# Kernel tuning notes

Measured on AMD Instinct MI355X. Metric: run time of the kernel, lower is better.

## Reference

```python
import jax, jax.numpy as jnp
import numpy as np

N_NODES = 100000
NEG_SLOPE = 0.2  # PyG GATConv default LeakyReLU slope


def gat_conv(x, W, att_src, att_dst, bias, edge_index, num_nodes, concat):
    """PyG-style GATConv with default add_self_loops=True.
    x: [N, Fin], W: [Fin, H*C], att_src/att_dst: [H, C], bias: [H*C] or [C].
    """
    H, C = att_src.shape
    h = (x @ W).reshape(num_nodes, H, C)              # [N, H, C]
    # append self-loops (PyG default)
    loops = jnp.arange(num_nodes, dtype=edge_index.dtype)
    src = jnp.concatenate([edge_index[0], loops])     # [E+N]
    dst = jnp.concatenate([edge_index[1], loops])
    # per-node attention logits, then per-edge score
    a_src = jnp.sum(h * att_src[None], axis=-1)       # [N, H]
    a_dst = jnp.sum(h * att_dst[None], axis=-1)       # [N, H]
    e = jax.nn.leaky_relu(a_src[src] + a_dst[dst], NEG_SLOPE)  # [E+N, H]
    # softmax over incoming edges of each destination node
    m = jax.ops.segment_max(e, dst, num_segments=num_nodes)    # [N, H]
    e = jnp.exp(e - m[dst])
    denom = jax.ops.segment_sum(e, dst, num_segments=num_nodes)
    alpha = e / denom[dst]                                      # [E+N, H]
    # scatter-aggregate weighted source features
    msg = h[src] * alpha[..., None]                             # [E+N, H, C]
    out = jax.ops.segment_sum(msg, dst, num_segments=num_nodes)  # [N, H, C]
    if concat:
        out = out.reshape(num_nodes, H * C)
    else:
        out = out.mean(axis=1)
    return out + bias


def setup_inputs() -> dict:
    key = jax.random.key(0)
    ks = jax.random.split(key, 12)
    N, E = N_NODES, 1600000
    Fin, Ch, Hh, Cout = 128, 64, 2, 64

    def glorot(k, shape):
        fan = shape[0] + shape[-1]
        return jax.random.uniform(k, shape, jnp.float32, -1.0, 1.0) * np.sqrt(6.0 / fan)

    x = jax.random.normal(ks[0], (N, Fin), jnp.float32)
    edge_index = jax.random.randint(ks[1], (2, E), 0, N, jnp.int32)
    W1 = glorot(ks[2], (Fin, Hh * Ch))
    att_src1 = glorot(ks[3], (Hh, Ch))
    att_dst1 = glorot(ks[4], (Hh, Ch))
    b1 = jnp.zeros((Hh * Ch,), jnp.float32)
    W2 = glorot(ks[5], (Hh * Ch, Cout))
    att_src2 = glorot(ks[6], (1, Cout))
    att_dst2 = glorot(ks[7], (1, Cout))
    b2 = jnp.zeros((Cout,), jnp.float32)
    return {"x": x, "edge_index": edge_index,
            "W1": W1, "att_src1": att_src1, "att_dst1": att_dst1, "b1": b1,
            "W2": W2, "att_src2": att_src2, "att_dst2": att_dst2, "b2": b2}


def reference(x, edge_index, W1, att_src1, att_dst1, b1, W2, att_src2, att_dst2, b2):
    h = gat_conv(x, W1, att_src1, att_dst1, b1, edge_index, N_NODES, concat=True)
    h = jax.nn.elu(h)
    out = gat_conv(h, W2, att_src2, att_dst2, b2, edge_index, N_NODES, concat=True)
    return out
```

## Files before the change

### kernel.cpp

```cpp
#include <hip/hip_runtime.h>
#include <hip/hip_bf16.h>
#include <cstdint>
#include <cstddef>

static constexpr int FIN = 128;
static constexpr int HC1 = 128;
static constexpr int EPB = 4096;

typedef __attribute__((ext_vector_type(8))) short short8;
typedef __attribute__((ext_vector_type(4))) float f32x4;

__device__ __forceinline__ float bf2f(unsigned int u) { return __uint_as_float(u << 16); }
__device__ __forceinline__ unsigned short f2bf(float f) {
  unsigned int u = __float_as_uint(f);
  return (unsigned short)((u + 0x7fff + ((u >> 16) & 1)) >> 16);
}
__device__ __forceinline__ float lrelu02(float x) { return x > 0.f ? x : 0.2f * x; }
__device__ __forceinline__ int rl_i(int v, int l) { return __builtin_amdgcn_readlane(v, l); }
__device__ __forceinline__ unsigned int q8b(float x, float inv) {
  float q = fminf(fmaxf(x * inv, -127.f), 127.f);
  return (unsigned int)((int)rintf(q) + 128) & 255u;
}
#define NEG_INF __int_as_float(0xff800000)

__global__ __launch_bounds__(256) void bucket_hist(const int* __restrict__ dst,
                                                   int* __restrict__ bhist, int E, int NB) {
  __shared__ int lh[512];
  int t = threadIdx.x;
  lh[t] = 0; lh[t + 256] = 0;
  __syncthreads();
  int e0 = blockIdx.x * EPB;
  #pragma unroll
  for (int i = 0; i < EPB / 256; i++) {
    int e = e0 + i * 256 + t;
    if (e < E) atomicAdd(&lh[dst[e] >> 8], 1);
  }
  __syncthreads();
  for (int x = t; x < NB; x += 256) {
    int c = lh[x];
    if (c > 0) atomicAdd(&bhist[x], c);
  }
}

__global__ __launch_bounds__(512) void scan_buckets(const int* __restrict__ bhist,
                                                    int* __restrict__ boffs, int n) {
  __shared__ int sh[512];
  int t = threadIdx.x;
  int v = (t < n) ? bhist[t] : 0;
  sh[t] = v; __syncthreads();
  for (int d = 1; d < 512; d <<= 1) {
    int w = (t >= d) ? sh[t - d] : 0;
    __syncthreads();
    sh[t] += w;
    __syncthreads();
  }
  if (t <= n) boffs[t] = sh[t] - v;
}

__global__ __launch_bounds__(256) void bucket_scatter(const int* __restrict__ src,
                                                      const int* __restrict__ dst,
                                                      const int* __restrict__ boffs,
                                                      int* __restrict__ gcur,
                                                      unsigned int* __restrict__ sorted,
                                                      int E, int NB) {
  __shared__ int lh[512];
  int t = threadIdx.x;
  lh[t] = 0; lh[t + 256] = 0;
  __syncthreads();
  int e0 = blockIdx.x * EPB;
  #pragma unroll
  for (int i = 0; i < EPB / 256; i++) {
    int e = e0 + i * 256 + t;
    if (e < E) atomicAdd(&lh[dst[e] >> 8], 1);
  }
  __syncthreads();
  for (int x = t; x < NB; x += 256) {
    int c = lh[x];
    lh[x] = (c > 0) ? (boffs[x] + atomicAdd(&gcur[x], c)) : 0;
  }
  __syncthreads();
  #pragma unroll
  for (int i = 0; i < EPB / 256; i++) {
    int e = e0 + i * 256 + t;
    if (e < E) {
      int d = dst[e];
      int pos = atomicAdd(&lh[d >> 8], 1);
      sorted[pos] = ((unsigned int)src[e] << 8) | (unsigned int)(d & 255);
    }
  }
}

__global__ __launch_bounds__(256) void bucket_count(const unsigned int* __restrict__ sorted,
                                                    const int* __restrict__ boffs,
                                                    int* __restrict__ counts, int N) {
  __shared__ int cnt[256];
  int b = blockIdx.x, t = threadIdx.x;
  cnt[t] = 0; __syncthreads();
  int beg = boffs[b], end = boffs[b + 1];
  for (int p = beg + t; p < end; p += 256)
    atomicAdd(&cnt[sorted[p] & 255u], 1);
  __syncthreads();
  int d = b * 256 + t;
  if (d < N) counts[d] = cnt[t];
}

__global__ __launch_bounds__(256) void scan_block(const int* __restrict__ cnt,
                                                  int* __restrict__ offs,
                                                  int* __restrict__ bsum, int n) {
  __shared__ int sh[256];
  int t = threadIdx.x;
  int i = blockIdx.x * 256 + t;
  int v = (i < n) ? cnt[i] : 0;
  sh[t] = v; __syncthreads();
  for (int d = 1; d < 256; d <<= 1) {
    int w = (t >= d) ? sh[t - d] : 0;
    __syncthreads();
    sh[t] += w;
    __syncthreads();
  }
  if (i < n) offs[i] = sh[t] - v;
  if (t == 255) bsum[blockIdx.x] = sh[255];
}

__global__ __launch_bounds__(512) void scan_top(int* __restrict__ bsum, int nb) {
  __shared__ int sh[512];
  int t = threadIdx.x;
  int v = (t < nb) ? bsum[t] : 0;
  sh[t] = v; __syncthreads();
  for (int d = 1; d < 512; d <<= 1) {
    int w = (t >= d) ? sh[t - d] : 0;
    __syncthreads();
    sh[t] += w;
    __syncthreads();
  }
  if (t < nb) bsum[t] = sh[t] - v;
}

__global__ __launch_bounds__(256) void scan_add(int* __restrict__ offs,
                                                const int* __restrict__ bsum, int n, int E) {
  int i = blockIdx.x * 256 + threadIdx.x;
  if (i < n) offs[i] += bsum[i >> 8];
  if (i == n) offs[n] = E;
}

__global__ __launch_bounds__(256) void bucket_place(const unsigned int* __restrict__ sorted,
                                                    const int* __restrict__ boffs,
                                                    const int* __restrict__ offs,
                                                    int* __restrict__ ssrc, int N) {
  __shared__ int offl[256];
  __shared__ int cur[256];
  int b = blockIdx.x, t = threadIdx.x;
  int d = b * 256 + t;
  offl[t] = (d < N) ? offs[d] : 0;
  cur[t] = 0;
  __syncthreads();
  int beg = boffs[b], end = boffs[b + 1];
  for (int p = beg + t; p < end; p += 256) {
    unsigned int pk = sorted[p];
    int dl = pk & 255u;
    int r = atomicAdd(&cur[dl], 1);
    ssrc[offl[dl] + r] = (int)(pk >> 8);
  }
}

template <int COLS, bool AF32>
__global__ __launch_bounds__(256) void gemm_mfma(const void* __restrict__ Av,
                                                 const float* __restrict__ Wv,
                                                 unsigned char* __restrict__ Cq,
                                                 float* __restrict__ scl,
                                                 int nrows) {
  constexpr int NT = COLS / 16;
  __shared__ unsigned short WT[COLS][136];
  __shared__ __align__(16) unsigned char pack[4][16 * COLS];

  const int tid = threadIdx.x;
  constexpr int NPC = COLS / 4;
  for (int idx = tid; idx < 128 * NPC; idx += 256) {
    int k = idx / NPC;
    int n0 = (idx - k * NPC) * 4;
    float4 wv = *(const float4*)(Wv + (size_t)k * COLS + n0);
    WT[n0 + 0][k] = f2bf(wv.x);
    WT[n0 + 1][k] = f2bf(wv.y);
    WT[n0 + 2][k] = f2bf(wv.z);
    WT[n0 + 3][k] = f2bf(wv.w);
  }
  __syncthreads();

  const int w = tid >> 6, lane = tid & 63;
  const int quad = lane >> 4, cl = lane & 15;
  const int rbase = blockIdx.x * 128 + w * 32;

  f32x4 acc[2][NT];
  #pragma unroll
  for (int rt = 0; rt < 2; rt++)
    #pragma unroll
    for (int ct = 0; ct < NT; ct++) acc[rt][ct] = (f32x4){0.f, 0.f, 0.f, 0.f};

  #pragma unroll
  for (int kc = 0; kc < 4; kc++) {
    const int k0 = kc * 32 + quad * 8;
    short8 a[2];
    #pragma unroll
    for (int rt = 0; rt < 2; rt++) {
      int row = rbase + rt * 16 + cl;
      row = min(row, nrows - 1);
      if constexpr (AF32) {
        const float* ap = (const float*)Av + (size_t)row * 128 + k0;
        float4 f0 = *(const float4*)ap;
        float4 f1 = *(const float4*)(ap + 4);
        short8 t;
        t[0] = (short)f2bf(f0.x); t[1] = (short)f2bf(f0.y);
        t[2] = (short)f2bf(f0.z); t[3] = (short)f2bf(f0.w);
        t[4] = (short)f2bf(f1.x); t[5] = (short)f2bf(f1.y);
        t[6] = (short)f2bf(f1.z); t[7] = (short)f2bf(f1.w);
        a[rt] = t;
      } else {
        a[rt] = *(const short8*)((const unsigned short*)Av + (size_t)row * 128 + k0);
      }
    }
    #pragma unroll
    for (int ct = 0; ct < NT; ct++) {
      short8 b = *(const short8*)&WT[ct * 16 + cl][k0];
      #pragma unroll
      for (int rt = 0; rt < 2; rt++)
        acc[rt][ct] = __builtin_amdgcn_mfma_f32_16x16x32_bf16(a[rt], b, acc[rt][ct], 0, 0, 0);
    }
  }

  #pragma unroll
  for (int rt = 0; rt < 2; rt++) {
    #pragma unroll
    for (int r = 0; r < 4; r++) {
      float mx = 0.f;
      #pragma unroll
      for (int ct = 0; ct < NT; ct++) mx = fmaxf(mx, fabsf(acc[rt][ct][r]));
      mx = fmaxf(mx, __shfl_xor(mx, 1));
      mx = fmaxf(mx, __shfl_xor(mx, 2));
      mx = fmaxf(mx, __shfl_xor(mx, 4));
      mx = fmaxf(mx, __shfl_xor(mx, 8));
      float inv = mx > 0.f ? 127.f / mx : 0.f;
      int grow = rbase + rt * 16 + quad * 4 + r;
      if (cl == 0 && grow < nrows) scl[grow] = mx * (1.f / 127.f);
      #pragma unroll
      for (int ct = 0; ct < NT; ct++)
        pack[w][(quad * 4 + r) * COLS + ct * 16 + cl] =
            (unsigned char)q8b(acc[rt][ct][r], inv);
    }
    __syncthreads();
    if constexpr (COLS == 128) {
      #pragma unroll
      for (int i = 0; i < 2; i++) {
        int off = i * 1024 + lane * 16;
        uint4 v = *(const uint4*)&pack[w][off];
        int grow = rbase + rt * 16 + (off >> 7);
        if (grow < nrows)
          *(uint4*)(Cq + (size_t)grow * 128 + (off & 127)) = v;
      }
    } else {
      int off = lane * 16;
      uint4 v = *(const uint4*)&pack[w][off];
      int grow = rbase + rt * 16 + (off >> 6);
      if (grow < nrows)
        *(uint4*)(Cq + (size_t)grow * 64 + (off & 63)) = v;
    }
    __syncthreads();
  }
}

template <int H>
__global__ __launch_bounds__(256) void attn_logits(const void* __restrict__ hq,
                                                   const float* __restrict__ scl,
                                                   const float* __restrict__ att_s,
                                                   const float* __restrict__ att_d,
                                                   float* __restrict__ asrc,
                                                   float* __restrict__ adst, int n) {
  int node = (int)((blockIdx.x * (unsigned)blockDim.x + threadIdx.x) >> 6);
  int lane = threadIdx.x & 63;
  if (node >= n) return;
  float sv = scl[node];
  float ss, sd;
  if constexpr (H == 2) {
    unsigned int v = ((const unsigned short*)hq)[(size_t)node * 64 + lane];
    float hv0 = (float)(v & 255u) - 128.f;
    float hv1 = (float)((v >> 8) & 255u) - 128.f;
    int ch = lane * 2;
    ss = hv0 * att_s[ch] + hv1 * att_s[ch + 1];
    sd = hv0 * att_d[ch] + hv1 * att_d[ch + 1];
  } else {
    float hv = (float)((const unsigned char*)hq)[(size_t)node * 64 + lane] - 128.f;
    ss = hv * att_s[lane];
    sd = hv * att_d[lane];
  }
  #pragma unroll
  for (int d = (H == 1 ? 32 : 16); d >= 1; d >>= 1) {
    ss += __shfl_xor(ss, d);
    sd += __shfl_xor(sd, d);
  }
  int gl = (H == 2) ? (lane & 31) : lane;
  int hd = (H == 2) ? (lane >> 5) : 0;
  if (gl == 0) {
    asrc[(size_t)node * H + hd] = ss * sv;
    adst[(size_t)node * H + hd] = sd * sv;
  }
}

template <int H, bool ELU_OUT, bool F32OUT>
__global__ __launch_bounds__(256) void agg_gather(const void* __restrict__ hq,
                                                  const float* __restrict__ scl,
                                                  const float* __restrict__ asrc,
                                                  const float* __restrict__ adst,
                                                  const int* __restrict__ offs,
                                                  const int* __restrict__ ssrc,
                                                  const float* __restrict__ bias,
                                                  void* __restrict__ outv, int n) {
  __shared__ float pshare[4][64];
  __shared__ int vshare[4][64];
  const int tid = threadIdx.x;
  const int wid = tid >> 6;
  int node = (int)((blockIdx.x * (unsigned)blockDim.x + tid) >> 6);
  int lane = tid & 63;
  if (node >= n) return;
  const int hd = lane >> 5;
  const int beg = offs[node], end = offs[node + 1];
  const unsigned short* hq16 = (const unsigned short*)hq;
  const unsigned char* hqb = (const unsigned char*)hq;

  float adh, m, acc0, acc1, d;
  float SPF = 0.f;
  const float s_self = scl[node];
  if constexpr (H == 2) {
    float2 adv = ((const float2*)adst)[node];
    float2 asv = ((const float2*)asrc)[node];
    adh = hd ? adv.y : adv.x;
    m = lrelu02((hd ? asv.y : asv.x) + adh);
    unsigned int v = hq16[((size_t)node << 6) + lane];
    acc0 = s_self * ((float)(v & 255u) - 128.f);
    acc1 = s_self * ((float)((v >> 8) & 255u) - 128.f);
  } else {
    adh = adst[node];
    m = lrelu02(asrc[node] + adh);
    if (hd == 0) {
      unsigned int v = hq16[((size_t)node << 5) + lane];
      acc0 = s_self * ((float)(v & 255u) - 128.f);
      acc1 = s_self * ((float)((v >> 8) & 255u) - 128.f);
    } else {
      acc0 = 0.f; acc1 = 0.f;
    }
  }
  d = 1.f;

  constexpr int CH = (H == 2) ? 32 : 64;
  const int lvoff = (lane & 31) * 2;
  for (int pos = beg; pos < end; pos += CH) {
    const int len = min(CH, end - pos);
    int li = (H == 2) ? (lane & 31) : lane;
    bool valid = li < len;
    int s_l = valid ? ssrc[pos + li] : 0;
    float scl_l = valid ? scl[s_l] : 0.f;
    float e_l;
    if constexpr (H == 2) {
      float a = asrc[(s_l << 1) + hd];
      e_l = valid ? lrelu02(a + adh) : NEG_INF;
    } else {
      float a = asrc[s_l];
      e_l = valid ? lrelu02(a + adh) : NEG_INF;
    }
    float mc = e_l;
    #pragma unroll
    for (int dlt = CH >> 1; dlt >= 1; dlt >>= 1) mc = fmaxf(mc, __shfl_xor(mc, dlt));
    float m_new = fmaxf(m, mc);
    float f = __expf(m - m_new);
    float p_l = __expf(e_l - m_new);
    float sc = p_l;
    #pragma unroll
    for (int dlt = CH >> 1; dlt >= 1; dlt >>= 1) sc += __shfl_xor(sc, dlt);
    d = d * f + sc;
    acc0 *= f; acc1 *= f;
    m = m_new;
    p_l *= scl_l;

    pshare[wid][lane] = p_l;
    float spf = p_l;
    if constexpr (H == 2) {
      #pragma unroll
      for (int dlt = 16; dlt >= 1; dlt >>= 1) spf += __shfl_xor(spf, dlt);
    } else {
      vshare[wid][lane] = s_l << 6;
      #pragma unroll
      for (int dlt = 32; dlt >= 1; dlt >>= 1) spf += __shfl_xor(spf, dlt);
    }
    SPF = SPF * f + spf;

    if constexpr (H == 2) {
      const int ng = (len + 7) >> 3;
      for (int g = 0; g < ng; g++) {
        const int jb = g * 8;
        unsigned short v[8];
        #pragma unroll
        for (int k = 0; k < 8; k++) {
          int s = rl_i(s_l, jb + k);
          v[k] = hq16[((size_t)(unsigned)s << 6) + lane];
        }
        float pv[8];
        #pragma unroll
        for (int k = 0; k < 8; k++) pv[k] = pshare[wid][hd * 32 + jb + k];
        #pragma unroll
        for (int k = 0; k < 8; k++) {
          unsigned int w = v[k];
          acc0 = fmaf(pv[k], (float)(w & 255u), acc0);
          acc1 = fmaf(pv[k], (float)((w >> 8) & 255u), acc1);
        }
      }
    } else {
      const int npair = (len + 1) >> 1;
      const int ng = (npair + 7) >> 3;
      for (int g = 0; g < ng; g++) {
        const int jb = g * 16;
        unsigned short v[8];
        #pragma unroll
        for (int k = 0; k < 8; k++) {
          int voff = vshare[wid][jb + 2 * k + hd];
          v[k] = *(const unsigned short*)(hqb + (unsigned)voff + lvoff);
        }
        float pv[8];
        #pragma unroll
        for (int k = 0; k < 8; k++) pv[k] = pshare[wid][jb + 2 * k + hd];
        #pragma unroll
        for (int k = 0; k < 8; k++) {
          unsigned int w = v[k];
          acc0 = fmaf(pv[k], (float)(w & 255u), acc0);
          acc1 = fmaf(pv[k], (float)((w >> 8) & 255u), acc1);
        }
      }
    }
  }

  if constexpr (H == 1) {
    acc0 += __shfl_xor(acc0, 32);
    acc1 += __shfl_xor(acc1, 32);
  }
  acc0 = fmaf(-128.f, SPF, acc0);
  acc1 = fmaf(-128.f, SPF, acc1);

  const float inv = 1.f / d;
  if constexpr (H == 2) {
    float2 bv = ((const float2*)bias)[lane];
    float v0 = acc0 * inv + bv.x;
    float v1 = acc1 * inv + bv.y;
    if (ELU_OUT) {
      v0 = v0 > 0.f ? v0 : (__expf(v0) - 1.f);
      v1 = v1 > 0.f ? v1 : (__expf(v1) - 1.f);
    }
    if constexpr (F32OUT) {
      ((float2*)outv)[(size_t)node * 64 + lane] = make_float2(v0, v1);
    } else {
      unsigned int pk = (unsigned int)f2bf(v0) | ((unsigned int)f2bf(v1) << 16);
      ((unsigned int*)outv)[(size_t)node * 64 + lane] = pk;
    }
  } else {
    if (hd == 0) {
      float2 bv = ((const float2*)bias)[lane];
      float v0 = acc0 * inv + bv.x;
      float v1 = acc1 * inv + bv.y;
      if (ELU_OUT) {
        v0 = v0 > 0.f ? v0 : (__expf(v0) - 1.f);
        v1 = v1 > 0.f ? v1 : (__expf(v1) - 1.f);
      }
      if constexpr (F32OUT) {
        ((float2*)outv)[(size_t)node * 32 + lane] = make_float2(v0, v1);
      } else {
        unsigned int pk = (unsigned int)f2bf(v0) | ((unsigned int)f2bf(v1) << 16);
        ((unsigned int*)outv)[(size_t)node * 32 + lane] = pk;
      }
    }
  }
}

extern "C" void kernel_launch(void* const* d_in, const int* in_sizes, int n_in,
                              void* d_out, int out_size, void* d_ws, size_t ws_size,
                              hipStream_t stream) {
  const int N = in_sizes[0] / FIN;
  const int E = in_sizes[1] / 2;

  const void*  x   = d_in[0];
  const int*   ei  = (const int*)d_in[1];
  const float* W1  = (const float*)d_in[2];
  const float* as1 = (const float*)d_in[3];
  const float* ad1 = (const float*)d_in[4];
  const float* b1  = (const float*)d_in[5];
  const float* W2  = (const float*)d_in[6];
  const float* as2 = (const float*)d_in[7];
  const float* ad2 = (const float*)d_in[8];
  const float* b2  = (const float*)d_in[9];

  const int* e_src = ei;
  const int* e_dst = ei + E;

  char* p = (char*)d_ws;
  auto carve = [&](size_t bytes) {
    char* q = p;
    p += (bytes + 255) & ~(size_t)255;
    return (void*)q;
  };
  unsigned char* h1q = (unsigned char*)carve((size_t)N * 128);
  float* scl1        = (float*)carve((size_t)N * 4);
  unsigned char* h2q = (unsigned char*)carve((size_t)N * 64);
  float* scl2        = (float*)carve((size_t)N * 4);
  unsigned short* buf2 = (unsigned short*)carve((size_t)N * HC1 * 2);
  float* asrc1 = (float*)carve((size_t)N * 2 * 4);
  float* adst1 = (float*)carve((size_t)N * 2 * 4);
  float* asrc2 = (float*)carve((size_t)N * 4);
  float* adst2 = (float*)carve((size_t)N * 4);
  int* counts  = (int*)carve((size_t)N * 4);
  int* offs    = (int*)carve((size_t)(N + 1) * 4);
  int* bsum    = (int*)carve(512 * 4);
  int* bhist   = (int*)carve((size_t)2 * 512 * 4);
  int* gcur    = bhist + 512;
  int* boffs   = (int*)carve(513 * 4);
  unsigned int* sorted = (unsigned int*)carve((size_t)E * 4);
  int* ssrc    = (int*)carve((size_t)E * 4);

  const int NB = (N + 255) >> 8;
  const int nb = (N + 255) / 256;
  const int sgrid = (E + EPB - 1) / EPB;
  const int wgrid = (int)(((size_t)N * 64 + 255) / 256);
  const int ggrid = (N + 127) / 128;

  hipMemsetAsync(bhist, 0, (size_t)2 * 512 * 4, stream);
  bucket_hist<<<sgrid, 256, 0, stream>>>(e_dst, bhist, E, NB);
  scan_buckets<<<1, 512, 0, stream>>>(bhist, boffs, NB);
  bucket_scatter<<<sgrid, 256, 0, stream>>>(e_src, e_dst, boffs, gcur, sorted, E, NB);
  bucket_count<<<NB, 256, 0, stream>>>(sorted, boffs, counts, N);
  scan_block<<<nb, 256, 0, stream>>>(counts, offs, bsum, N);
  scan_top<<<1, 512, 0, stream>>>(bsum, nb);
  scan_add<<<(N + 256) / 256, 256, 0, stream>>>(offs, bsum, N, E);
  bucket_place<<<NB, 256, 0, stream>>>(sorted, boffs, offs, ssrc, N);

  gemm_mfma<128, true><<<ggrid, 256, 0, stream>>>(x, W1, h1q, scl1, N);
  attn_logits<2><<<wgrid, 256, 0, stream>>>(h1q, scl1, as1, ad1, asrc1, adst1, N);
  agg_gather<2, true, false><<<wgrid, 256, 0, stream>>>(h1q, scl1, asrc1, adst1, offs, ssrc,
                                                        b1, buf2, N);

  gemm_mfma<64, false><<<ggrid, 256, 0, stream>>>(buf2, W2, h2q, scl2, N);
  attn_logits<1><<<wgrid, 256, 0, stream>>>(h2q, scl2, as2, ad2, asrc2, adst2, N);
  agg_gather<1, false, true><<<wgrid, 256, 0, stream>>>(h2q, scl2, asrc2, adst2, offs, ssrc,
                                                        b2, d_out, N);
}
```

Baseline: 346.0 us.

## Fuse CSR offset scan into bucket placement and attention logits into GEMM epilogue

Replaces the count/scan_block/scan_top/scan_add/place kernel chain with one per-bucket kernel. It works because each bucket covers 256 destinations and its global start is already known from the bucket offsets, so a local prefix scan is enough. It also computes the per-node source and destination attention logits inside the MFMA GEMM epilogue from the fp32 accumulators, which removes the separate attn_logits kernels and their re-read of the quantized features. This cuts five kernel launches and some global traffic, at the cost of extra shuffles and registers in the GEMM epilogue. As a side effect the logits now come from unquantized values.

Measured after the change: 310.3 us. 1.12x faster.

```diff
diff --git a/kernel.cpp b/kernel.cpp
--- a/kernel.cpp
+++ b/kernel.cpp
@@ -90,86 +90,54 @@
   }
 }
 
-__global__ __launch_bounds__(256) void bucket_count(const unsigned int* __restrict__ sorted,
-                                                    const int* __restrict__ boffs,
-                                                    int* __restrict__ counts, int N) {
+__global__ __launch_bounds__(256) void bucket_place_fused(const unsigned int* __restrict__ sorted,
+                                                          const int* __restrict__ boffs,
+                                                          int* __restrict__ offs,
+                                                          int* __restrict__ ssrc,
+                                                          int N, int E) {
   __shared__ int cnt[256];
+  __shared__ int pref[256];
   int b = blockIdx.x, t = threadIdx.x;
-  cnt[t] = 0; __syncthreads();
+  cnt[t] = 0;
+  __syncthreads();
   int beg = boffs[b], end = boffs[b + 1];
   for (int p = beg + t; p < end; p += 256)
     atomicAdd(&cnt[sorted[p] & 255u], 1);
   __syncthreads();
-  int d = b * 256 + t;
-  if (d < N) counts[d] = cnt[t];
-}
-
-__global__ __launch_bounds__(256) void scan_block(const int* __restrict__ cnt,
-                                                  int* __restrict__ offs,
-                                                  int* __restrict__ bsum, int n) {
-  __shared__ int sh[256];
-  int t = threadIdx.x;
-  int i = blockIdx.x * 256 + t;
-  int v = (i < n) ? cnt[i] : 0;
-  sh[t] = v; __syncthreads();
+  int v = cnt[t];
+  pref[t] = v; __syncthreads();
   for (int d = 1; d < 256; d <<= 1) {
-    int w = (t >= d) ? sh[t - d] : 0;
+    int w = (t >= d) ? pref[t - d] : 0;
     __syncthreads();
-    sh[t] += w;
+    pref[t] += w;
     __syncthreads();
   }
-  if (i < n) offs[i] = sh[t] - v;
-  if (t == 255) bsum[blockIdx.x] = sh[255];
-}
-
-__global__ __launch_bounds__(512) void scan_top(int* __restrict__ bsum, int nb) {
-  __shared__ int sh[512];
-  int t = threadIdx.x;
-  int v = (t < nb) ? bsum[t] : 0;
-  sh[t] = v; __syncthreads();
-  for (int d = 1; d < 512; d <<= 1) {
-    int w = (t >= d) ? sh[t - d] : 0;
-    __syncthreads();
-    sh[t] += w;
-    __syncthreads();
-  }
-  if (t < nb) bsum[t] = sh[t] - v;
-}
-
-__global__ __launch_bounds__(256) void scan_add(int* __restrict__ offs,
-                                                const int* __restrict__ bsum, int n, int E) {
-  int i = blockIdx.x * 256 + threadIdx.x;
-  if (i < n) offs[i] += bsum[i >> 8];
-  if (i == n) offs[n] = E;
-}
-
-__global__ __launch_bounds__(256) void bucket_place(const unsigned int* __restrict__ sorted,
-                                                    const int* __restrict__ boffs,
-                                                    const int* __restrict__ offs,
-                                                    int* __restrict__ ssrc, int N) {
-  __shared__ int offl[256];
-  __shared__ int cur[256];
-  int b = blockIdx.x, t = threadIdx.x;
-  int d = b * 256 + t;
-  offl[t] = (d < N) ? offs[d] : 0;
-  cur[t] = 0;
-  __syncthreads();
-  int beg = boffs[b], end = boffs[b + 1];
+  int excl = pref[t] - v;
+  int node = b * 256 + t;
+  if (node < N) offs[node] = beg + excl;
+  if (b == 0 && t == 0) offs[N] = E;
+  cnt[t] = beg + excl;
+  __syncthreads();
   for (int p = beg + t; p < end; p += 256) {
     unsigned int pk = sorted[p];
     int dl = pk & 255u;
-    int r = atomicAdd(&cur[dl], 1);
-    ssrc[offl[dl] + r] = (int)(pk >> 8);
+    int r = atomicAdd(&cnt[dl], 1);
+    ssrc[r] = (int)(pk >> 8);
   }
 }
 
 template <int COLS, bool AF32>
 __global__ __launch_bounds__(256) void gemm_mfma(const void* __restrict__ Av,
                                                  const float* __restrict__ Wv,
+                                                 const float* __restrict__ att_s,
+                                                 const float* __restrict__ att_d,
                                                  unsigned char* __restrict__ Cq,
                                                  float* __restrict__ scl,
+                                                 float* __restrict__ asrc,
+                                                 float* __restrict__ adst,
                                                  int nrows) {
   constexpr int NT = COLS / 16;
+  constexpr int H = COLS / 64;
   __shared__ unsigned short WT[COLS][136];
   __shared__ __align__(16) unsigned char pack[4][16 * COLS];
 
@@ -184,11 +152,18 @@
     WT[n0 + 2][k] = f2bf(wv.z);
     WT[n0 + 3][k] = f2bf(wv.w);
   }
-  __syncthreads();
 
   const int w = tid >> 6, lane = tid & 63;
   const int quad = lane >> 4, cl = lane & 15;
   const int rbase = blockIdx.x * 128 + w * 32;
+
+  float asv[NT], adv[NT];
+  #pragma unroll
+  for (int ct = 0; ct < NT; ct++) {
+    asv[ct] = att_s[ct * 16 + cl];
+    adv[ct] = att_d[ct * 16 + cl];
+  }
+  __syncthreads();
 
   f32x4 acc[2][NT];
   #pragma unroll
@@ -231,16 +206,42 @@
   for (int rt = 0; rt < 2; rt++) {
     #pragma unroll
     for (int r = 0; r < 4; r++) {
+      int grow = rbase + rt * 16 + quad * 4 + r;
+      float s0 = 0.f, s1 = 0.f, d0 = 0.f, d1 = 0.f;
       float mx = 0.f;
       #pragma unroll
-      for (int ct = 0; ct < NT; ct++) mx = fmaxf(mx, fabsf(acc[rt][ct][r]));
-      mx = fmaxf(mx, __shfl_xor(mx, 1));
-      mx = fmaxf(mx, __shfl_xor(mx, 2));
-      mx = fmaxf(mx, __shfl_xor(mx, 4));
-      mx = fmaxf(mx, __shfl_xor(mx, 8));
+      for (int ct = 0; ct < NT; ct++) {
+        float av = acc[rt][ct][r];
+        mx = fmaxf(mx, fabsf(av));
+        if (H == 2 && ct >= NT / 2) {
+          s1 = fmaf(av, asv[ct], s1);
+          d1 = fmaf(av, adv[ct], d1);
+        } else {
+          s0 = fmaf(av, asv[ct], s0);
+          d0 = fmaf(av, adv[ct], d0);
+        }
+      }
+      #pragma unroll
+      for (int dd = 8; dd >= 1; dd >>= 1) {
+        mx = fmaxf(mx, __shfl_xor(mx, dd));
+        s0 += __shfl_xor(s0, dd);
+        d0 += __shfl_xor(d0, dd);
+        if (H == 2) {
+          s1 += __shfl_xor(s1, dd);
+          d1 += __shfl_xor(d1, dd);
+        }
+      }
       float inv = mx > 0.f ? 127.f / mx : 0.f;
-      int grow = rbase + rt * 16 + quad * 4 + r;
-      if (cl == 0 && grow < nrows) scl[grow] = mx * (1.f / 127.f);
+      if (cl == 0 && grow < nrows) {
+        scl[grow] = mx * (1.f / 127.f);
+        if (H == 2) {
+          ((float2*)asrc)[grow] = make_float2(s0, s1);
+          ((float2*)adst)[grow] = make_float2(d0, d1);
+        } else {
+          asrc[grow] = s0;
+          adst[grow] = d0;
+        }
+      }
       #pragma unroll
       for (int ct = 0; ct < NT; ct++)
         pack[w][(quad * 4 + r) * COLS + ct * 16 + cl] =
@@ -264,43 +265,6 @@
         *(uint4*)(Cq + (size_t)grow * 64 + (off & 63)) = v;
     }
     __syncthreads();
-  }
-}
-
-template <int H>
-__global__ __launch_bounds__(256) void attn_logits(const void* __restrict__ hq,
-                                                   const float* __restrict__ scl,
-                                                   const float* __restrict__ att_s,
-                                                   const float* __restrict__ att_d,
-                                                   float* __restrict__ asrc,
-                                                   float* __restrict__ adst, int n) {
-  int node = (int)((blockIdx.x * (unsigned)blockDim.x + threadIdx.x) >> 6);
-  int lane = threadIdx.x & 63;
-  if (node >= n) return;
-  float sv = scl[node];
-  float ss, sd;
-  if constexpr (H == 2) {
-    unsigned int v = ((const unsigned short*)hq)[(size_t)node * 64 + lane];
-    float hv0 = (float)(v & 255u) - 128.f;
-    float hv1 = (float)((v >> 8) & 255u) - 128.f;
-    int ch = lane * 2;
-    ss = hv0 * att_s[ch] + hv1 * att_s[ch + 1];
-    sd = hv0 * att_d[ch] + hv1 * att_d[ch + 1];
-  } else {
-    float hv = (float)((const unsigned char*)hq)[(size_t)node * 64 + lane] - 128.f;
-    ss = hv * att_s[lane];
-    sd = hv * att_d[lane];
-  }
-  #pragma unroll
-  for (int d = (H == 1 ? 32 : 16); d >= 1; d >>= 1) {
-    ss += __shfl_xor(ss, d);
-    sd += __shfl_xor(sd, d);
-  }
-  int gl = (H == 2) ? (lane & 31) : lane;
-  int hd = (H == 2) ? (lane >> 5) : 0;
-  if (gl == 0) {
-    asrc[(size_t)node * H + hd] = ss * sv;
-    adst[(size_t)node * H + hd] = sd * sv;
   }
 }
 
@@ -511,9 +475,7 @@
   float* adst1 = (float*)carve((size_t)N * 2 * 4);
   float* asrc2 = (float*)carve((size_t)N * 4);
   float* adst2 = (float*)carve((size_t)N * 4);
-  int* counts  = (int*)carve((size_t)N * 4);
   int* offs    = (int*)carve((size_t)(N + 1) * 4);
-  int* bsum    = (int*)carve(512 * 4);
   int* bhist   = (int*)carve((size_t)2 * 512 * 4);
   int* gcur    = bhist + 512;
   int* boffs   = (int*)carve(513 * 4);
@@ -521,7 +483,6 @@
   int* ssrc    = (int*)carve((size_t)E * 4);
 
   const int NB = (N + 255) >> 8;
-  const int nb = (N + 255) / 256;
   const int sgrid = (E + EPB - 1) / EPB;
   const int wgrid = (int)(((size_t)N * 64 + 255) / 256);
   const int ggrid = (N + 127) / 128;
@@ -530,19 +491,15 @@
   bucket_hist<<<sgrid, 256, 0, stream>>>(e_dst, bhist, E, NB);
   scan_buckets<<<1, 512, 0, stream>>>(bhist, boffs, NB);
   bucket_scatter<<<sgrid, 256, 0, stream>>>(e_src, e_dst, boffs, gcur, sorted, E, NB);
-  bucket_count<<<NB, 256, 0, stream>>>(sorted, boffs, counts, N);
-  scan_block<<<nb, 256, 0, stream>>>(counts, offs, bsum, N);
-  scan_top<<<1, 512, 0, stream>>>(bsum, nb);
-  scan_add<<<(N + 256) / 256, 256, 0, stream>>>(offs, bsum, N, E);
-  bucket_place<<<NB, 256, 0, stream>>>(sorted, boffs, offs, ssrc, N);
-
-  gemm_mfma<128, true><<<ggrid, 256, 0, stream>>>(x, W1, h1q, scl1, N);
-  attn_logits<2><<<wgrid, 256, 0, stream>>>(h1q, scl1, as1, ad1, asrc1, adst1, N);
+  bucket_place_fused<<<NB, 256, 0, stream>>>(sorted, boffs, offs, ssrc, N, E);
+
+  gemm_mfma<128, true><<<ggrid, 256, 0, stream>>>(x, W1, as1, ad1, h1q, scl1,
+                                                  asrc1, adst1, N);
   agg_gather<2, true, false><<<wgrid, 256, 0, stream>>>(h1q, scl1, asrc1, adst1, offs, ssrc,
                                                         b1, buf2, N);
 
-  gemm_mfma<64, false><<<ggrid, 256, 0, stream>>>(buf2, W2, h2q, scl2, N);
-  attn_logits<1><<<wgrid, 256, 0, stream>>>(h2q, scl2, as2, ad2, asrc2, adst2, N);
+  gemm_mfma<64, false><<<ggrid, 256, 0, stream>>>(buf2, W2, as2, ad2, h2q, scl2,
+                                                  asrc2, adst2, N);
   agg_gather<1, false, true><<<wgrid, 256, 0, stream>>>(h2q, scl2, asrc2, adst2, offs, ssrc,
                                                         b2, d_out, N);
 }
```
